# Kernel tuning notes

Measured on AMD Instinct MI355X. Metric: run time of the kernel, lower is better.

## Reference

```python
import jax, jax.numpy as jnp
import numpy as np

N, E, D = 50000, 600000, 128


def setup_inputs() -> dict:
    key = jax.random.key(0)
    ks = jax.random.split(key, 16)
    s = 0.05
    inp = {
        "x": jax.random.normal(ks[0], (N, D), dtype=jnp.float32),
        "Wv": jax.random.normal(ks[1], (D, D), dtype=jnp.float32) * s,
        "bv": jnp.zeros((D,), dtype=jnp.float32),
        "Wa": jax.random.normal(ks[2], (D, D), dtype=jnp.float32) * s,
        "ba": jnp.zeros((D,), dtype=jnp.float32),
        "Wm1": jax.random.normal(ks[3], (D, D), dtype=jnp.float32) * s,
        "bm1": jnp.zeros((D,), dtype=jnp.float32),
        "Wm2": jax.random.normal(ks[4], (D, D), dtype=jnp.float32) * s,
        "bm2": jnp.zeros((D,), dtype=jnp.float32),
        "Wp1": jax.random.normal(ks[5], (D, D), dtype=jnp.float32) * s,
        "bp1": jnp.zeros((D,), dtype=jnp.float32),
        "Wp2": jax.random.normal(ks[6], (D, D), dtype=jnp.float32) * s,
        "bp2": jnp.zeros((D,), dtype=jnp.float32),
        "edge_index": jax.random.randint(ks[7], (2, E), 0, N, dtype=jnp.int64),
        "batch": jnp.zeros((N,), dtype=jnp.int64),
        "passes": 4,
    }
    return inp


def reference(x, Wv, bv, Wa, ba, Wm1, bm1, Wm2, bm2, Wp1, bp1, Wp2, bp2,
              edge_index, batch, passes):
    src, dst = edge_index[0], edge_index[1]
    n = x.shape[0]
    h = x
    for _ in range(passes):
        # gather source features, sum-aggregate at destination nodes
        aggr = jax.ops.segment_sum(h[src], dst, num_segments=n)  # [N, D]
        # update: V(h) + min(h, A(aggr)); V/A are Linear+ReLU (1-layer MLP)
        upd = jax.nn.relu(h @ Wv + bv) + jnp.minimum(h, jax.nn.relu(aggr @ Wa + ba))
        # combine MLP (2 layers: Linear-ReLU-Linear)
        upd = jax.nn.relu(upd @ Wm1 + bm1) @ Wm2 + bm2
        h = jax.nn.relu(upd)
    # final prediction: two stacked Linears, no activation between
    return (h @ Wp1 + bp1) @ Wp2 + bp2
```

## Files before the change

kernel.cpp:

```cpp
#include <hip/hip_runtime.h>

#define D 128

typedef _Float16 half8 __attribute__((ext_vector_type(8)));
typedef float f32x4 __attribute__((ext_vector_type(4)));

__device__ __forceinline__ float frelu(float x) { return fmaxf(x, 0.f); }

__global__ void count_kernel(const int* __restrict__ dst, int E, int* __restrict__ deg) {
    int e = blockIdx.x * blockDim.x + threadIdx.x;
    if (e < E) atomicAdd(&deg[dst[e]], 1);
}

__global__ void scan_partial(const int* __restrict__ deg, int* __restrict__ bsum, int n) {
    __shared__ int red[256];
    int i = blockIdx.x * 256 + threadIdx.x;
    red[threadIdx.x] = (i < n) ? deg[i] : 0;
    __syncthreads();
#pragma unroll
    for (int off = 128; off > 0; off >>= 1) {
        if (threadIdx.x < off) red[threadIdx.x] += red[threadIdx.x + off];
        __syncthreads();
    }
    if (threadIdx.x == 0) bsum[blockIdx.x] = red[0];
}

__global__ void scan_bsum(const int* __restrict__ bsum, int* __restrict__ bpre,
                          int* __restrict__ rowstart, int nb, int n) {
    __shared__ int s[256];
    int t = threadIdx.x;
    int v = (t < nb) ? bsum[t] : 0;
    s[t] = v;
    __syncthreads();
#pragma unroll
    for (int off = 1; off < 256; off <<= 1) {
        int u = 0;
        if (t >= off) u = s[t - off];
        __syncthreads();
        if (t >= off) s[t] += u;
        __syncthreads();
    }
    if (t < nb) bpre[t] = s[t] - v;
    if (t == 255) rowstart[n] = s[255];
}

__global__ void scan_expand(const int* __restrict__ deg, const int* __restrict__ bpre,
                            int* __restrict__ rowstart, int n) {
    __shared__ int s[256];
    int b = blockIdx.x, t = threadIdx.x;
    int i = b * 256 + t;
    int v = (i < n) ? deg[i] : 0;
    s[t] = v;
    __syncthreads();
#pragma unroll
    for (int off = 1; off < 256; off <<= 1) {
        int u = 0;
        if (t >= off) u = s[t - off];
        __syncthreads();
        if (t >= off) s[t] += u;
        __syncthreads();
    }
    if (i < n) rowstart[i] = bpre[b] + s[t] - v;
}

__global__ void fill_kernel(const int* __restrict__ src, const int* __restrict__ dst, int E,
                            const int* __restrict__ rowstart, int* __restrict__ cursor,
                            int* __restrict__ bucket) {
    int e = blockIdx.x * blockDim.x + threadIdx.x;
    if (e < E) {
        int d = dst[e];
        int pos = atomicAdd(&cursor[d], 1);
        bucket[rowstart[d] + pos] = src[e];
    }
}

__global__ void gather_kernel(const float* __restrict__ h, const int* __restrict__ rowstart,
                              const int* __restrict__ bucket, float* __restrict__ aggr, int n) {
    int node = blockIdx.x * 4 + (threadIdx.x >> 6);
    if (node >= n) return;
    int lane = threadIdx.x & 63;
    int col = lane & 31, hf = lane >> 5;
    const float4* __restrict__ h4 = reinterpret_cast<const float4*>(h);
    int s = rowstart[node], e = rowstart[node + 1];
    float4 a[8];
#pragma unroll
    for (int m = 0; m < 8; ++m) a[m] = float4{0.f, 0.f, 0.f, 0.f};
    int j = s;
    for (; j + 16 <= e; j += 16) {
#pragma unroll
        for (int m = 0; m < 8; ++m) {
            float4 v = h4[(size_t)bucket[j + 2 * m + hf] * 32 + col];
            a[m].x += v.x; a[m].y += v.y; a[m].z += v.z; a[m].w += v.w;
        }
    }
    for (; j + 2 <= e; j += 2) {
        float4 v = h4[(size_t)bucket[j + hf] * 32 + col];
        a[0].x += v.x; a[0].y += v.y; a[0].z += v.z; a[0].w += v.w;
    }
    if (j < e && hf == 0) {
        float4 v = h4[(size_t)bucket[j] * 32 + col];
        a[0].x += v.x; a[0].y += v.y; a[0].z += v.z; a[0].w += v.w;
    }
    float4 r;
    r.x = ((a[0].x + a[1].x) + (a[2].x + a[3].x)) + ((a[4].x + a[5].x) + (a[6].x + a[7].x));
    r.y = ((a[0].y + a[1].y) + (a[2].y + a[3].y)) + ((a[4].y + a[5].y) + (a[6].y + a[7].y));
    r.z = ((a[0].z + a[1].z) + (a[2].z + a[3].z)) + ((a[4].z + a[5].z) + (a[6].z + a[7].z));
    r.w = ((a[0].w + a[1].w) + (a[2].w + a[3].w)) + ((a[4].w + a[5].w) + (a[6].w + a[7].w));
    r.x += __shfl(r.x, lane ^ 32);
    r.y += __shfl(r.y, lane ^ 32);
    r.z += __shfl(r.z, lane ^ 32);
    r.w += __shfl(r.w, lane ^ 32);
    if (hf == 0)
        reinterpret_cast<float4*>(aggr)[(size_t)node * 32 + col] = r;
}

__global__ void pack_kernel(const float* __restrict__ W0, const float* __restrict__ W1,
                            const float* __restrict__ W2, const float* __restrict__ W3,
                            const float* __restrict__ W4, const float* __restrict__ W5,
                            _Float16* __restrict__ pk) {
    const float* Ws[6] = {W0, W1, W2, W3, W4, W5};
    const float* __restrict__ W = Ws[blockIdx.x];
    half8* __restrict__ base = reinterpret_cast<half8*>(pk) + (size_t)blockIdx.x * 4096;
    for (int it = threadIdx.x; it < 2048; it += 256) {
        int lane = it & 63, ks = (it >> 6) & 3, cf = it >> 8;
        int c = cf * 16 + (lane & 15);
        half8 hv, lv;
#pragma unroll
        for (int e = 0; e < 8; ++e) {
            int k = ks * 32 + ((e < 4) ? 0 : 16) + (lane >> 4) * 4 + (e & 3);
            float w = W[k * 128 + c];
            _Float16 hi = (_Float16)w;
            hv[e] = hi;
            lv[e] = (_Float16)(w - (float)hi);
        }
        base[(cf * 4 + ks) * 64 + lane] = hv;
        base[2048 + (cf * 4 + ks) * 64 + lane] = lv;
    }
}


__device__ __forceinline__ void split8(const float4 x0, const float4 x1, half8& hh, half8& ll) {
    float xs[8] = {x0.x, x0.y, x0.z, x0.w, x1.x, x1.y, x1.z, x1.w};
#pragma unroll
    for (int e = 0; e < 8; ++e) {
        _Float16 hi = (_Float16)xs[e];
        hh[e] = hi;
        ll[e] = (_Float16)(xs[e] - (float)hi);
    }
}

enum { M_P1, M_P2, M_RELU_BAND, M_RELU_GLOB, M_BIAS_BAND, M_BIAS_GLOB };

#define MFMA(acc, A, B) acc = __builtin_amdgcn_mfma_f32_16x16x32_f16((A), (B), acc, 0, 0, 0)

template <int MODE>
__device__ __forceinline__ void do_cf(int cf,
                                      const half8 ah[4], const half8 al[4],
                                      const half8 bh[4], const half8 bl[4],
                                      float* __restrict__ sB,
                                      const float* __restrict__ bias,
                                      const float* __restrict__ hsrc,
                                      float* __restrict__ gout,
                                      int lane, int band0, int n) {
    const int cl = lane & 15;
    const int lrb = (lane >> 4) * 4;
    f32x4 a0 = {0.f, 0.f, 0.f, 0.f}, a1 = {0.f, 0.f, 0.f, 0.f};
    MFMA(a0, ah[0], bh[0]); MFMA(a0, al[0], bh[0]); MFMA(a0, ah[0], bl[0]); MFMA(a0, al[0], bl[0]);
    MFMA(a0, ah[1], bh[1]); MFMA(a0, al[1], bh[1]); MFMA(a0, ah[1], bl[1]); MFMA(a0, al[1], bl[1]);
    MFMA(a1, ah[2], bh[2]); MFMA(a1, al[2], bh[2]); MFMA(a1, ah[2], bl[2]); MFMA(a1, al[2], bl[2]);
    MFMA(a1, ah[3], bh[3]); MFMA(a1, al[3], bh[3]); MFMA(a1, ah[3], bl[3]); MFMA(a1, al[3], bl[3]);

    const float bb = bias[cf * 16 + cl];
    const int c = cf * 16 + cl;
    const int cq = c >> 2, cr = c & 3;
#pragma unroll
    for (int g = 0; g < 4; ++g) {
        const int r = lrb + g;
        const int slot = cq ^ (r & 7);
        float* __restrict__ addr = &sB[r * 128 + slot * 4 + cr];
        float v = a0[g] + a1[g] + bb;
        if constexpr (MODE == M_P1) {
            *addr = frelu(v);
        } else if constexpr (MODE == M_P2) {
            float u1 = *addr;
            int gr = band0 + r;
            float hv = (gr < n) ? hsrc[(size_t)gr * D + c] : 0.f;
            *addr = frelu(v) + fminf(hv, u1);
        } else if constexpr (MODE == M_RELU_BAND) {
            *addr = frelu(v);
        } else if constexpr (MODE == M_BIAS_BAND) {
            *addr = v;
        } else if constexpr (MODE == M_RELU_GLOB) {
            int gr = band0 + r;
            if (gr < n) gout[(size_t)gr * D + c] = frelu(v);
        } else {
            int gr = band0 + r;
            if (gr < n) gout[(size_t)gr * D + c] = v;
        }
    }
}

template <int MODE, bool A_GLOBAL>
__device__ __forceinline__ void phase(const float4* __restrict__ Ag,
                                      float4* __restrict__ B4,
                                      float* __restrict__ sB,
                                      const half8* __restrict__ pkm,
                                      const float* __restrict__ bias,
                                      const float* __restrict__ hsrc,
                                      float* __restrict__ gout,
                                      int lane, int band0, int n) {
    const int lr = lane & 15;
    const int kb = lane >> 4;

    half8 ah[4], al[4];
    if constexpr (A_GLOBAL) {
        const float4 z = {0.f, 0.f, 0.f, 0.f};
        const int row = band0 + lr;
        const float4* __restrict__ base = Ag + (size_t)row * 32;
        const bool ok = row < n;
#pragma unroll
        for (int ks = 0; ks < 4; ++ks) {
            float4 x0 = ok ? base[ks * 8 + kb] : z;
            float4 x1 = ok ? base[ks * 8 + 4 + kb] : z;
            split8(x0, x1, ah[ks], al[ks]);
        }
    } else {
        const int key = lr & 7;
#pragma unroll
        for (int ks = 0; ks < 4; ++ks) {
            float4 x0 = B4[lr * 32 + ((ks * 8 + kb) ^ key)];
            float4 x1 = B4[lr * 32 + ((ks * 8 + 4 + kb) ^ key)];
            split8(x0, x1, ah[ks], al[ks]);
        }
    }

    const half8* __restrict__ ph = pkm;
    const half8* __restrict__ pl = pkm + 2048;

    half8 bh0[4], bl0[4], bh1[4], bl1[4];
#pragma unroll
    for (int ks = 0; ks < 4; ++ks) {
        bh0[ks] = ph[ks * 64 + lane];
        bl0[ks] = pl[ks * 64 + lane];
    }
#pragma unroll 1
    for (int cf2 = 0; cf2 < 4; ++cf2) {
        const int cfe = cf2 * 2, cfo = cfe + 1;
#pragma unroll
        for (int ks = 0; ks < 4; ++ks) {
            bh1[ks] = ph[(cfo * 4 + ks) * 64 + lane];
            bl1[ks] = pl[(cfo * 4 + ks) * 64 + lane];
        }
        do_cf<MODE>(cfe, ah, al, bh0, bl0, sB, bias, hsrc, gout, lane, band0, n);
        if (cf2 < 3) {
#pragma unroll
            for (int ks = 0; ks < 4; ++ks) {
                bh0[ks] = ph[((cfe + 2) * 4 + ks) * 64 + lane];
                bl0[ks] = pl[((cfe + 2) * 4 + ks) * 64 + lane];
            }
        }
        do_cf<MODE>(cfo, ah, al, bh1, bl1, sB, bias, hsrc, gout, lane, band0, n);
    }
}

__launch_bounds__(64)
__global__ void update_kernel(const float* __restrict__ h, const float* __restrict__ aggr,
                              const _Float16* __restrict__ pk,
                              const float* __restrict__ bv, const float* __restrict__ ba,
                              const float* __restrict__ bm1, const float* __restrict__ bm2,
                              float* __restrict__ hout, int n) {
    __shared__ float4 B4[512];
    float* sB = reinterpret_cast<float*>(B4);
    const int lane = threadIdx.x;
    const int band0 = blockIdx.x * 16;
    const half8* __restrict__ pk8 = reinterpret_cast<const half8*>(pk);
    const float4* __restrict__ h4 = reinterpret_cast<const float4*>(h);
    const float4* __restrict__ a4 = reinterpret_cast<const float4*>(aggr);

    phase<M_P1, true>(a4, B4, sB, pk8 + 0 * 4096, ba, nullptr, nullptr, lane, band0, n);
    phase<M_P2, true>(h4, B4, sB, pk8 + 1 * 4096, bv, h, nullptr, lane, band0, n);
    phase<M_RELU_BAND, false>(nullptr, B4, sB, pk8 + 2 * 4096, bm1, nullptr, nullptr, lane, band0, n);
    phase<M_RELU_GLOB, false>(nullptr, B4, sB, pk8 + 3 * 4096, bm2, nullptr, hout, lane, band0, n);
}

__launch_bounds__(64)
__global__ void final_kernel(const float* __restrict__ h, const _Float16* __restrict__ pk,
                             const float* __restrict__ bp1, const float* __restrict__ bp2,
                             float* __restrict__ out, int n) {
    __shared__ float4 B4[512];
    float* sB = reinterpret_cast<float*>(B4);
    const int lane = threadIdx.x;
    const int band0 = blockIdx.x * 16;
    const half8* __restrict__ pk8 = reinterpret_cast<const half8*>(pk);
    const float4* __restrict__ h4 = reinterpret_cast<const float4*>(h);

    phase<M_BIAS_BAND, true>(h4, B4, sB, pk8 + 4 * 4096, bp1, nullptr, nullptr, lane, band0, n);
    phase<M_BIAS_GLOB, false>(nullptr, B4, sB, pk8 + 5 * 4096, bp2, nullptr, out, lane, band0, n);
}

extern "C" void kernel_launch(void* const* d_in, const int* in_sizes, int n_in,
                              void* d_out, int out_size, void* d_ws, size_t ws_size,
                              hipStream_t stream) {
    const float* x   = (const float*)d_in[0];
    const float* Wv  = (const float*)d_in[1];
    const float* bv  = (const float*)d_in[2];
    const float* Wa  = (const float*)d_in[3];
    const float* ba  = (const float*)d_in[4];
    const float* Wm1 = (const float*)d_in[5];
    const float* bm1 = (const float*)d_in[6];
    const float* Wm2 = (const float*)d_in[7];
    const float* bm2 = (const float*)d_in[8];
    const float* Wp1 = (const float*)d_in[9];
    const float* bp1 = (const float*)d_in[10];
    const float* Wp2 = (const float*)d_in[11];
    const float* bp2 = (const float*)d_in[12];
    const int* ei    = (const int*)d_in[13];

    const int N = in_sizes[0] / D;
    const int E = in_sizes[13] / 2;
    const int* src = ei;
    const int* dst = ei + E;

    char* ws = (char*)d_ws;
    size_t off = 0;
    auto alloc = [&](size_t bytes) -> void* {
        void* p = ws + off;
        off += (bytes + 255) & ~(size_t)255;
        return p;
    };
    float* hb0  = (float*)alloc((size_t)N * D * sizeof(float));
    float* hb1  = (float*)alloc((size_t)N * D * sizeof(float));
    float* aggr = (float*)alloc((size_t)N * D * sizeof(float));
    int* deg      = (int*)alloc((size_t)(N + 1) * sizeof(int));
    int* rowstart = (int*)alloc((size_t)(N + 1) * sizeof(int));
    int* cursor   = (int*)alloc((size_t)(N + 1) * sizeof(int));
    int* bucket   = (int*)alloc((size_t)E * sizeof(int));
    int* bsum     = (int*)alloc(256 * sizeof(int));
    int* bpre     = (int*)alloc(256 * sizeof(int));
    _Float16* pk  = (_Float16*)alloc((size_t)6 * 2 * 128 * 128 * sizeof(_Float16));

    hipMemsetAsync(deg, 0, (size_t)(N + 1) * sizeof(int), stream);
    hipMemsetAsync(cursor, 0, (size_t)(N + 1) * sizeof(int), stream);

    pack_kernel<<<6, 256, 0, stream>>>(Wa, Wv, Wm1, Wm2, Wp1, Wp2, pk);

    int eb = (E + 255) / 256;
    int nb = (N + 255) / 256;
    count_kernel<<<eb, 256, 0, stream>>>(dst, E, deg);
    scan_partial<<<nb, 256, 0, stream>>>(deg, bsum, N);
    scan_bsum<<<1, 256, 0, stream>>>(bsum, bpre, rowstart, nb, N);
    scan_expand<<<nb, 256, 0, stream>>>(deg, bpre, rowstart, N);
    fill_kernel<<<eb, 256, 0, stream>>>(src, dst, E, rowstart, cursor, bucket);

    int ub = (N + 15) / 16;
    int gb = (N + 3) / 4;
    const float* cur = x;
    float* bufs[2] = {hb0, hb1};
    for (int p = 0; p < 4; ++p) {
        gather_kernel<<<gb, 256, 0, stream>>>(cur, rowstart, bucket, aggr, N);
        float* nxt = bufs[p & 1];
        update_kernel<<<ub, 64, 0, stream>>>(cur, aggr, pk, bv, ba, bm1, bm2, nxt, N);
        cur = nxt;
    }
    final_kernel<<<ub, 64, 0, stream>>>(cur, pk, bp1, bp2, (float*)d_out, N);
}
```

Measured before the change: 575.4 us.

## Process two 16-row bands per wavefront to reuse weight fragments across MFMAs

Result: faster. 550.9 us, median of 2 (-4.3%).

```diff
diff --git a/kernel.cpp b/kernel.cpp
--- a/kernel.cpp
+++ b/kernel.cpp
@@ -154,36 +154,27 @@
 #define MFMA(acc, A, B) acc = __builtin_amdgcn_mfma_f32_16x16x32_f16((A), (B), acc, 0, 0, 0)
 
 template <int MODE>
-__device__ __forceinline__ void do_cf(int cf,
-                                      const half8 ah[4], const half8 al[4],
-                                      const half8 bh[4], const half8 bl[4],
-                                      float* __restrict__ sB,
-                                      const float* __restrict__ bias,
-                                      const float* __restrict__ hsrc,
-                                      float* __restrict__ gout,
-                                      int lane, int band0, int n) {
+__device__ __forceinline__ void epi_band(float v4[4], int b, int cf,
+                                         float* __restrict__ sB,
+                                         const float* __restrict__ hsrc,
+                                         float* __restrict__ gout,
+                                         int lane, int row0, int n, float bb) {
     const int cl = lane & 15;
     const int lrb = (lane >> 4) * 4;
-    f32x4 a0 = {0.f, 0.f, 0.f, 0.f}, a1 = {0.f, 0.f, 0.f, 0.f};
-    MFMA(a0, ah[0], bh[0]); MFMA(a0, al[0], bh[0]); MFMA(a0, ah[0], bl[0]); MFMA(a0, al[0], bl[0]);
-    MFMA(a0, ah[1], bh[1]); MFMA(a0, al[1], bh[1]); MFMA(a0, ah[1], bl[1]); MFMA(a0, al[1], bl[1]);
-    MFMA(a1, ah[2], bh[2]); MFMA(a1, al[2], bh[2]); MFMA(a1, ah[2], bl[2]); MFMA(a1, al[2], bl[2]);
-    MFMA(a1, ah[3], bh[3]); MFMA(a1, al[3], bh[3]); MFMA(a1, ah[3], bl[3]); MFMA(a1, al[3], bl[3]);
-
-    const float bb = bias[cf * 16 + cl];
     const int c = cf * 16 + cl;
     const int cq = c >> 2, cr = c & 3;
+    float* __restrict__ sBb = sB + b * 2048;
 #pragma unroll
     for (int g = 0; g < 4; ++g) {
         const int r = lrb + g;
         const int slot = cq ^ (r & 7);
-        float* __restrict__ addr = &sB[r * 128 + slot * 4 + cr];
-        float v = a0[g] + a1[g] + bb;
+        float* __restrict__ addr = &sBb[r * 128 + slot * 4 + cr];
+        float v = v4[g] + bb;
         if constexpr (MODE == M_P1) {
             *addr = frelu(v);
         } else if constexpr (MODE == M_P2) {
             float u1 = *addr;
-            int gr = band0 + r;
+            int gr = row0 + b * 16 + r;
             float hv = (gr < n) ? hsrc[(size_t)gr * D + c] : 0.f;
             *addr = frelu(v) + fminf(hv, u1);
         } else if constexpr (MODE == M_RELU_BAND) {
@@ -191,13 +182,49 @@
         } else if constexpr (MODE == M_BIAS_BAND) {
             *addr = v;
         } else if constexpr (MODE == M_RELU_GLOB) {
-            int gr = band0 + r;
+            int gr = row0 + b * 16 + r;
             if (gr < n) gout[(size_t)gr * D + c] = frelu(v);
         } else {
-            int gr = band0 + r;
+            int gr = row0 + b * 16 + r;
             if (gr < n) gout[(size_t)gr * D + c] = v;
         }
     }
+}
+
+template <int MODE>
+__device__ __forceinline__ void do_cf(int cf,
+                                      const half8 ah0[4], const half8 al0[4],
+                                      const half8 ah1[4], const half8 al1[4],
+                                      const half8 bh[4], const half8 bl[4],
+                                      float* __restrict__ sB,
+                                      const float* __restrict__ bias,
+                                      const float* __restrict__ hsrc,
+                                      float* __restrict__ gout,
+                                      int lane, int row0, int n) {
+    f32x4 p0 = {0.f, 0.f, 0.f, 0.f}, p1 = {0.f, 0.f, 0.f, 0.f};
+    f32x4 q0 = {0.f, 0.f, 0.f, 0.f}, q1 = {0.f, 0.f, 0.f, 0.f};
+    MFMA(p0, ah0[0], bh[0]); MFMA(q0, ah1[0], bh[0]);
+    MFMA(p0, al0[0], bh[0]); MFMA(q0, al1[0], bh[0]);
+    MFMA(p0, ah0[0], bl[0]); MFMA(q0, ah1[0], bl[0]);
+    MFMA(p0, al0[0], bl[0]); MFMA(q0, al1[0], bl[0]);
+    MFMA(p0, ah0[1], bh[1]); MFMA(q0, ah1[1], bh[1]);
+    MFMA(p0, al0[1], bh[1]); MFMA(q0, al1[1], bh[1]);
+    MFMA(p0, ah0[1], bl[1]); MFMA(q0, ah1[1], bl[1]);
+    MFMA(p0, al0[1], bl[1]); MFMA(q0, al1[1], bl[1]);
+    MFMA(p1, ah0[2], bh[2]); MFMA(q1, ah1[2], bh[2]);
+    MFMA(p1, al0[2], bh[2]); MFMA(q1, al1[2], bh[2]);
+    MFMA(p1, ah0[2], bl[2]); MFMA(q1, ah1[2], bl[2]);
+    MFMA(p1, al0[2], bl[2]); MFMA(q1, al1[2], bl[2]);
+    MFMA(p1, ah0[3], bh[3]); MFMA(q1, ah1[3], bh[3]);
+    MFMA(p1, al0[3], bh[3]); MFMA(q1, al1[3], bh[3]);
+    MFMA(p1, ah0[3], bl[3]); MFMA(q1, ah1[3], bl[3]);
+    MFMA(p1, al0[3], bl[3]); MFMA(q1, al1[3], bl[3]);
+
+    const float bb = bias[cf * 16 + (lane & 15)];
+    float v0[4] = {p0[0] + p1[0], p0[1] + p1[1], p0[2] + p1[2], p0[3] + p1[3]};
+    float v1[4] = {q0[0] + q1[0], q0[1] + q1[1], q0[2] + q1[2], q0[3] + q1[3]};
+    epi_band<MODE>(v0, 0, cf, sB, hsrc, gout, lane, row0, n, bb);
+    epi_band<MODE>(v1, 1, cf, sB, hsrc, gout, lane, row0, n, bb);
 }
 
 template <int MODE, bool A_GLOBAL>
@@ -208,21 +235,25 @@
                                       const float* __restrict__ bias,
                                       const float* __restrict__ hsrc,
                                       float* __restrict__ gout,
-                                      int lane, int band0, int n) {
+                                      int lane, int row0, int n) {
     const int lr = lane & 15;
     const int kb = lane >> 4;
 
-    half8 ah[4], al[4];
+    half8 ah0[4], al0[4], ah1[4], al1[4];
     if constexpr (A_GLOBAL) {
         const float4 z = {0.f, 0.f, 0.f, 0.f};
-        const int row = band0 + lr;
-        const float4* __restrict__ base = Ag + (size_t)row * 32;
-        const bool ok = row < n;
+        const int r0 = row0 + lr, r1 = row0 + 16 + lr;
+        const float4* __restrict__ b0 = Ag + (size_t)r0 * 32;
+        const float4* __restrict__ b1 = Ag + (size_t)r1 * 32;
+        const bool ok0 = r0 < n, ok1 = r1 < n;
 #pragma unroll
         for (int ks = 0; ks < 4; ++ks) {
-            float4 x0 = ok ? base[ks * 8 + kb] : z;
-            float4 x1 = ok ? base[ks * 8 + 4 + kb] : z;
-            split8(x0, x1, ah[ks], al[ks]);
+            float4 x0 = ok0 ? b0[ks * 8 + kb] : z;
+            float4 x1 = ok0 ? b0[ks * 8 + 4 + kb] : z;
+            split8(x0, x1, ah0[ks], al0[ks]);
+            float4 y0 = ok1 ? b1[ks * 8 + kb] : z;
+            float4 y1 = ok1 ? b1[ks * 8 + 4 + kb] : z;
+            split8(y0, y1, ah1[ks], al1[ks]);
         }
     } else {
         const int key = lr & 7;
@@ -230,7 +261,10 @@
         for (int ks = 0; ks < 4; ++ks) {
             float4 x0 = B4[lr * 32 + ((ks * 8 + kb) ^ key)];
             float4 x1 = B4[lr * 32 + ((ks * 8 + 4 + kb) ^ key)];
-            split8(x0, x1, ah[ks], al[ks]);
+            split8(x0, x1, ah0[ks], al0[ks]);
+            float4 y0 = B4[512 + lr * 32 + ((ks * 8 + kb) ^ key)];
+            float4 y1 = B4[512 + lr * 32 + ((ks * 8 + 4 + kb) ^ key)];
+            split8(y0, y1, ah1[ks], al1[ks]);
         }
     }
 
@@ -251,7 +285,7 @@
             bh1[ks] = ph[(cfo * 4 + ks) * 64 + lane];
             bl1[ks] = pl[(cfo * 4 + ks) * 64 + lane];
         }
-        do_cf<MODE>(cfe, ah, al, bh0, bl0, sB, bias, hsrc, gout, lane, band0, n);
+        do_cf<MODE>(cfe, ah0, al0, ah1, al1, bh0, bl0, sB, bias, hsrc, gout, lane, row0, n);
         if (cf2 < 3) {
 #pragma unroll
             for (int ks = 0; ks < 4; ++ks) {
@@ -259,7 +293,7 @@
                 bl0[ks] = pl[((cfe + 2) * 4 + ks) * 64 + lane];
             }
         }
-        do_cf<MODE>(cfo, ah, al, bh1, bl1, sB, bias, hsrc, gout, lane, band0, n);
+        do_cf<MODE>(cfo, ah0, al0, ah1, al1, bh1, bl1, sB, bias, hsrc, gout, lane, row0, n);
     }
 }
 
@@ -269,33 +303,33 @@
                               const float* __restrict__ bv, const float* __restrict__ ba,
                               const float* __restrict__ bm1, const float* __restrict__ bm2,
                               float* __restrict__ hout, int n) {
-    __shared__ float4 B4[512];
+    __shared__ float4 B4[1024];
     float* sB = reinterpret_cast<float*>(B4);
     const int lane = threadIdx.x;
-    const int band0 = blockIdx.x * 16;
+    const int row0 = blockIdx.x * 32;
     const half8* __restrict__ pk8 = reinterpret_cast<const half8*>(pk);
     const float4* __restrict__ h4 = reinterpret_cast<const float4*>(h);
     const float4* __restrict__ a4 = reinterpret_cast<const float4*>(aggr);
 
-    phase<M_P1, true>(a4, B4, sB, pk8 + 0 * 4096, ba, nullptr, nullptr, lane, band0, n);
-    phase<M_P2, true>(h4, B4, sB, pk8 + 1 * 4096, bv, h, nullptr, lane, band0, n);
-    phase<M_RELU_BAND, false>(nullptr, B4, sB, pk8 + 2 * 4096, bm1, nullptr, nullptr, lane, band0, n);
-    phase<M_RELU_GLOB, false>(nullptr, B4, sB, pk8 + 3 * 4096, bm2, nullptr, hout, lane, band0, n);
+    phase<M_P1, true>(a4, B4, sB, pk8 + 0 * 4096, ba, nullptr, nullptr, lane, row0, n);
+    phase<M_P2, true>(h4, B4, sB, pk8 + 1 * 4096, bv, h, nullptr, lane, row0, n);
+    phase<M_RELU_BAND, false>(nullptr, B4, sB, pk8 + 2 * 4096, bm1, nullptr, nullptr, lane, row0, n);
+    phase<M_RELU_GLOB, false>(nullptr, B4, sB, pk8 + 3 * 4096, bm2, nullptr, hout, lane, row0, n);
 }
 
 __launch_bounds__(64)
 __global__ void final_kernel(const float* __restrict__ h, const _Float16* __restrict__ pk,
                              const float* __restrict__ bp1, const float* __restrict__ bp2,
                              float* __restrict__ out, int n) {
-    __shared__ float4 B4[512];
+    __shared__ float4 B4[1024];
     float* sB = reinterpret_cast<float*>(B4);
     const int lane = threadIdx.x;
-    const int band0 = blockIdx.x * 16;
+    const int row0 = blockIdx.x * 32;
     const half8* __restrict__ pk8 = reinterpret_cast<const half8*>(pk);
     const float4* __restrict__ h4 = reinterpret_cast<const float4*>(h);
 
-    phase<M_BIAS_BAND, true>(h4, B4, sB, pk8 + 4 * 4096, bp1, nullptr, nullptr, lane, band0, n);
-    phase<M_BIAS_GLOB, false>(nullptr, B4, sB, pk8 + 5 * 4096, bp2, nullptr, out, lane, band0, n);
+    phase<M_BIAS_BAND, true>(h4, B4, sB, pk8 + 4 * 4096, bp1, nullptr, nullptr, lane, row0, n);
+    phase<M_BIAS_GLOB, false>(nullptr, B4, sB, pk8 + 5 * 4096, bp2, nullptr, out, lane, row0, n);
 }
 
 extern "C" void kernel_launch(void* const* d_in, const int* in_sizes, int n_in,
@@ -352,7 +386,7 @@
     scan_expand<<<nb, 256, 0, stream>>>(deg, bpre, rowstart, N);
     fill_kernel<<<eb, 256, 0, stream>>>(src, dst, E, rowstart, cursor, bucket);
 
-    int ub = (N + 15) / 16;
+    int ub = (N + 31) / 32;
     int gb = (N + 3) / 4;
     const float* cur = x;
     float* bufs[2] = {hb0, hb1};
```

## Split each 16-row band's output columns across four waves per block

Applied to the files above, without the earlier changes.

New measurement: 837.2 us. 1.45x slower.

```diff
diff --git a/kernel.cpp b/kernel.cpp
--- a/kernel.cpp
+++ b/kernel.cpp
@@ -157,11 +157,11 @@
 __device__ __forceinline__ void do_cf(int cf,
                                       const half8 ah[4], const half8 al[4],
                                       const half8 bh[4], const half8 bl[4],
-                                      float* __restrict__ sB,
+                                      float* __restrict__ sBw,
                                       const float* __restrict__ bias,
                                       const float* __restrict__ hsrc,
                                       float* __restrict__ gout,
-                                      int lane, int band0, int n) {
+                                      int lane, int row0, int n) {
     const int cl = lane & 15;
     const int lrb = (lane >> 4) * 4;
     f32x4 a0 = {0.f, 0.f, 0.f, 0.f}, a1 = {0.f, 0.f, 0.f, 0.f};
@@ -177,13 +177,13 @@
     for (int g = 0; g < 4; ++g) {
         const int r = lrb + g;
         const int slot = cq ^ (r & 7);
-        float* __restrict__ addr = &sB[r * 128 + slot * 4 + cr];
+        float* __restrict__ addr = &sBw[r * 128 + slot * 4 + cr];
         float v = a0[g] + a1[g] + bb;
         if constexpr (MODE == M_P1) {
             *addr = frelu(v);
         } else if constexpr (MODE == M_P2) {
             float u1 = *addr;
-            int gr = band0 + r;
+            int gr = row0 + r;
             float hv = (gr < n) ? hsrc[(size_t)gr * D + c] : 0.f;
             *addr = frelu(v) + fminf(hv, u1);
         } else if constexpr (MODE == M_RELU_BAND) {
@@ -191,31 +191,31 @@
         } else if constexpr (MODE == M_BIAS_BAND) {
             *addr = v;
         } else if constexpr (MODE == M_RELU_GLOB) {
-            int gr = band0 + r;
+            int gr = row0 + r;
             if (gr < n) gout[(size_t)gr * D + c] = frelu(v);
         } else {
-            int gr = band0 + r;
+            int gr = row0 + r;
             if (gr < n) gout[(size_t)gr * D + c] = v;
         }
     }
 }
 
 template <int MODE, bool A_GLOBAL>
-__device__ __forceinline__ void phase(const float4* __restrict__ Ag,
-                                      float4* __restrict__ B4,
-                                      float* __restrict__ sB,
-                                      const half8* __restrict__ pkm,
-                                      const float* __restrict__ bias,
-                                      const float* __restrict__ hsrc,
-                                      float* __restrict__ gout,
-                                      int lane, int band0, int n) {
+__device__ __forceinline__ void phaseW(const float4* __restrict__ Ag,
+                                       const float4* __restrict__ B4r,
+                                       float* __restrict__ sBw,
+                                       const half8* __restrict__ pkm,
+                                       const float* __restrict__ bias,
+                                       const float* __restrict__ hsrc,
+                                       float* __restrict__ gout,
+                                       int lane, int wv, int row0, int n) {
     const int lr = lane & 15;
     const int kb = lane >> 4;
 
     half8 ah[4], al[4];
     if constexpr (A_GLOBAL) {
         const float4 z = {0.f, 0.f, 0.f, 0.f};
-        const int row = band0 + lr;
+        const int row = row0 + lr;
         const float4* __restrict__ base = Ag + (size_t)row * 32;
         const bool ok = row < n;
 #pragma unroll
@@ -228,74 +228,70 @@
         const int key = lr & 7;
 #pragma unroll
         for (int ks = 0; ks < 4; ++ks) {
-            float4 x0 = B4[lr * 32 + ((ks * 8 + kb) ^ key)];
-            float4 x1 = B4[lr * 32 + ((ks * 8 + 4 + kb) ^ key)];
+            float4 x0 = B4r[lr * 32 + ((ks * 8 + kb) ^ key)];
+            float4 x1 = B4r[lr * 32 + ((ks * 8 + 4 + kb) ^ key)];
             split8(x0, x1, ah[ks], al[ks]);
         }
     }
 
     const half8* __restrict__ ph = pkm;
     const half8* __restrict__ pl = pkm + 2048;
-
-    half8 bh0[4], bl0[4], bh1[4], bl1[4];
+    const int cfA = wv * 2, cfB = cfA + 1;
+
+    half8 bhA[4], blA[4], bhB[4], blB[4];
 #pragma unroll
     for (int ks = 0; ks < 4; ++ks) {
-        bh0[ks] = ph[ks * 64 + lane];
-        bl0[ks] = pl[ks * 64 + lane];
-    }
-#pragma unroll 1
-    for (int cf2 = 0; cf2 < 4; ++cf2) {
-        const int cfe = cf2 * 2, cfo = cfe + 1;
-#pragma unroll
-        for (int ks = 0; ks < 4; ++ks) {
-            bh1[ks] = ph[(cfo * 4 + ks) * 64 + lane];
-            bl1[ks] = pl[(cfo * 4 + ks) * 64 + lane];
-        }
-        do_cf<MODE>(cfe, ah, al, bh0, bl0, sB, bias, hsrc, gout, lane, band0, n);
-        if (cf2 < 3) {
-#pragma unroll
-            for (int ks = 0; ks < 4; ++ks) {
-                bh0[ks] = ph[((cfe + 2) * 4 + ks) * 64 + lane];
-                bl0[ks] = pl[((cfe + 2) * 4 + ks) * 64 + lane];
-            }
-        }
-        do_cf<MODE>(cfo, ah, al, bh1, bl1, sB, bias, hsrc, gout, lane, band0, n);
-    }
-}
-
-__launch_bounds__(64)
+        bhA[ks] = ph[(cfA * 4 + ks) * 64 + lane];
+        blA[ks] = pl[(cfA * 4 + ks) * 64 + lane];
+        bhB[ks] = ph[(cfB * 4 + ks) * 64 + lane];
+        blB[ks] = pl[(cfB * 4 + ks) * 64 + lane];
+    }
+    do_cf<MODE>(cfA, ah, al, bhA, blA, sBw, bias, hsrc, gout, lane, row0, n);
+    do_cf<MODE>(cfB, ah, al, bhB, blB, sBw, bias, hsrc, gout, lane, row0, n);
+}
+
+__launch_bounds__(256)
 __global__ void update_kernel(const float* __restrict__ h, const float* __restrict__ aggr,
                               const _Float16* __restrict__ pk,
                               const float* __restrict__ bv, const float* __restrict__ ba,
                               const float* __restrict__ bm1, const float* __restrict__ bm2,
                               float* __restrict__ hout, int n) {
-    __shared__ float4 B4[512];
-    float* sB = reinterpret_cast<float*>(B4);
-    const int lane = threadIdx.x;
-    const int band0 = blockIdx.x * 16;
+    __shared__ float4 buf1[512];
+    __shared__ float4 buf2[512];
+    float* sB1 = reinterpret_cast<float*>(buf1);
+    float* sB2 = reinterpret_cast<float*>(buf2);
+    const int tid = threadIdx.x;
+    const int lane = tid & 63;
+    const int wv = tid >> 6;
+    const int row0 = blockIdx.x * 16;
     const half8* __restrict__ pk8 = reinterpret_cast<const half8*>(pk);
     const float4* __restrict__ h4 = reinterpret_cast<const float4*>(h);
     const float4* __restrict__ a4 = reinterpret_cast<const float4*>(aggr);
 
-    phase<M_P1, true>(a4, B4, sB, pk8 + 0 * 4096, ba, nullptr, nullptr, lane, band0, n);
-    phase<M_P2, true>(h4, B4, sB, pk8 + 1 * 4096, bv, h, nullptr, lane, band0, n);
-    phase<M_RELU_BAND, false>(nullptr, B4, sB, pk8 + 2 * 4096, bm1, nullptr, nullptr, lane, band0, n);
-    phase<M_RELU_GLOB, false>(nullptr, B4, sB, pk8 + 3 * 4096, bm2, nullptr, hout, lane, band0, n);
-}
-
-__launch_bounds__(64)
+    phaseW<M_P1, true>(a4, nullptr, sB1, pk8 + 0 * 4096, ba, nullptr, nullptr, lane, wv, row0, n);
+    phaseW<M_P2, true>(h4, nullptr, sB1, pk8 + 1 * 4096, bv, h, nullptr, lane, wv, row0, n);
+    __syncthreads();
+    phaseW<M_RELU_BAND, false>(nullptr, buf1, sB2, pk8 + 2 * 4096, bm1, nullptr, nullptr, lane, wv, row0, n);
+    __syncthreads();
+    phaseW<M_RELU_GLOB, false>(nullptr, buf2, nullptr, pk8 + 3 * 4096, bm2, nullptr, hout, lane, wv, row0, n);
+}
+
+__launch_bounds__(256)
 __global__ void final_kernel(const float* __restrict__ h, const _Float16* __restrict__ pk,
                              const float* __restrict__ bp1, const float* __restrict__ bp2,
                              float* __restrict__ out, int n) {
-    __shared__ float4 B4[512];
-    float* sB = reinterpret_cast<float*>(B4);
-    const int lane = threadIdx.x;
-    const int band0 = blockIdx.x * 16;
+    __shared__ float4 buf1[512];
+    float* sB1 = reinterpret_cast<float*>(buf1);
+    const int tid = threadIdx.x;
+    const int lane = tid & 63;
+    const int wv = tid >> 6;
+    const int row0 = blockIdx.x * 16;
     const half8* __restrict__ pk8 = reinterpret_cast<const half8*>(pk);
     const float4* __restrict__ h4 = reinterpret_cast<const float4*>(h);
 
-    phase<M_BIAS_BAND, true>(h4, B4, sB, pk8 + 4 * 4096, bp1, nullptr, nullptr, lane, band0, n);
-    phase<M_BIAS_GLOB, false>(nullptr, B4, sB, pk8 + 5 * 4096, bp2, nullptr, out, lane, band0, n);
+    phaseW<M_BIAS_BAND, true>(h4, nullptr, sB1, pk8 + 4 * 4096, bp1, nullptr, nullptr, lane, wv, row0, n);
+    __syncthreads();
+    phaseW<M_BIAS_GLOB, false>(nullptr, buf1, nullptr, pk8 + 5 * 4096, bp2, nullptr, out, lane, wv, row0, n);
 }
 
 extern "C" void kernel_launch(void* const* d_in, const int* in_sizes, int n_in,
@@ -359,8 +355,8 @@
     for (int p = 0; p < 4; ++p) {
         gather_kernel<<<gb, 256, 0, stream>>>(cur, rowstart, bucket, aggr, N);
         float* nxt = bufs[p & 1];
-        update_kernel<<<ub, 64, 0, stream>>>(cur, aggr, pk, bv, ba, bm1, bm2, nxt, N);
+        update_kernel<<<ub, 256, 0, stream>>>(cur, aggr, pk, bv, ba, bm1, bm2, nxt, N);
         cur = nxt;
     }
-    final_kernel<<<ub, 64, 0, stream>>>(cur, pk, bp1, bp2, (float*)d_out, N);
-}
+    final_kernel<<<ub, 256, 0, stream>>>(cur, pk, bp1, bp2, (float*)d_out, N);
+}
```

## Stage packed weights in LDS and share across eight waves per block

Applied to the files above, without the earlier changes.

New measurement: 592.6 us. 3.0% more time.

```diff
diff --git a/kernel.cpp b/kernel.cpp
--- a/kernel.cpp
+++ b/kernel.cpp
@@ -153,15 +153,21 @@
 
 #define MFMA(acc, A, B) acc = __builtin_amdgcn_mfma_f32_16x16x32_f16((A), (B), acc, 0, 0, 0)
 
+__device__ __forceinline__ void stageW(half8* __restrict__ sW,
+                                       const half8* __restrict__ pkm, int tid) {
+#pragma unroll
+    for (int i = 0; i < 8; ++i) sW[tid + i * 512] = pkm[tid + i * 512];
+}
+
 template <int MODE>
 __device__ __forceinline__ void do_cf(int cf,
                                       const half8 ah[4], const half8 al[4],
                                       const half8 bh[4], const half8 bl[4],
-                                      float* __restrict__ sB,
+                                      float* __restrict__ sBw,
                                       const float* __restrict__ bias,
                                       const float* __restrict__ hsrc,
                                       float* __restrict__ gout,
-                                      int lane, int band0, int n) {
+                                      int lane, int row0, int n) {
     const int cl = lane & 15;
     const int lrb = (lane >> 4) * 4;
     f32x4 a0 = {0.f, 0.f, 0.f, 0.f}, a1 = {0.f, 0.f, 0.f, 0.f};
@@ -177,13 +183,13 @@
     for (int g = 0; g < 4; ++g) {
         const int r = lrb + g;
         const int slot = cq ^ (r & 7);
-        float* __restrict__ addr = &sB[r * 128 + slot * 4 + cr];
+        float* __restrict__ addr = &sBw[r * 128 + slot * 4 + cr];
         float v = a0[g] + a1[g] + bb;
         if constexpr (MODE == M_P1) {
             *addr = frelu(v);
         } else if constexpr (MODE == M_P2) {
             float u1 = *addr;
-            int gr = band0 + r;
+            int gr = row0 + r;
             float hv = (gr < n) ? hsrc[(size_t)gr * D + c] : 0.f;
             *addr = frelu(v) + fminf(hv, u1);
         } else if constexpr (MODE == M_RELU_BAND) {
@@ -191,10 +197,10 @@
         } else if constexpr (MODE == M_BIAS_BAND) {
             *addr = v;
         } else if constexpr (MODE == M_RELU_GLOB) {
-            int gr = band0 + r;
+            int gr = row0 + r;
             if (gr < n) gout[(size_t)gr * D + c] = frelu(v);
         } else {
-            int gr = band0 + r;
+            int gr = row0 + r;
             if (gr < n) gout[(size_t)gr * D + c] = v;
         }
     }
@@ -202,20 +208,20 @@
 
 template <int MODE, bool A_GLOBAL>
 __device__ __forceinline__ void phase(const float4* __restrict__ Ag,
-                                      float4* __restrict__ B4,
+                                      const float4* __restrict__ B4,
                                       float* __restrict__ sB,
-                                      const half8* __restrict__ pkm,
+                                      const half8* __restrict__ sW,
                                       const float* __restrict__ bias,
                                       const float* __restrict__ hsrc,
                                       float* __restrict__ gout,
-                                      int lane, int band0, int n) {
+                                      int lane, int row0, int n) {
     const int lr = lane & 15;
     const int kb = lane >> 4;
 
     half8 ah[4], al[4];
     if constexpr (A_GLOBAL) {
         const float4 z = {0.f, 0.f, 0.f, 0.f};
-        const int row = band0 + lr;
+        const int row = row0 + lr;
         const float4* __restrict__ base = Ag + (size_t)row * 32;
         const bool ok = row < n;
 #pragma unroll
@@ -234,8 +240,8 @@
         }
     }
 
-    const half8* __restrict__ ph = pkm;
-    const half8* __restrict__ pl = pkm + 2048;
+    const half8* __restrict__ ph = sW;
+    const half8* __restrict__ pl = sW + 2048;
 
     half8 bh0[4], bl0[4], bh1[4], bl1[4];
 #pragma unroll
@@ -251,7 +257,7 @@
             bh1[ks] = ph[(cfo * 4 + ks) * 64 + lane];
             bl1[ks] = pl[(cfo * 4 + ks) * 64 + lane];
         }
-        do_cf<MODE>(cfe, ah, al, bh0, bl0, sB, bias, hsrc, gout, lane, band0, n);
+        do_cf<MODE>(cfe, ah, al, bh0, bl0, sB, bias, hsrc, gout, lane, row0, n);
         if (cf2 < 3) {
 #pragma unroll
             for (int ks = 0; ks < 4; ++ks) {
@@ -259,43 +265,67 @@
                 bl0[ks] = pl[((cfe + 2) * 4 + ks) * 64 + lane];
             }
         }
-        do_cf<MODE>(cfo, ah, al, bh1, bl1, sB, bias, hsrc, gout, lane, band0, n);
-    }
-}
-
-__launch_bounds__(64)
+        do_cf<MODE>(cfo, ah, al, bh1, bl1, sB, bias, hsrc, gout, lane, row0, n);
+    }
+}
+
+__launch_bounds__(512)
 __global__ void update_kernel(const float* __restrict__ h, const float* __restrict__ aggr,
                               const _Float16* __restrict__ pk,
                               const float* __restrict__ bv, const float* __restrict__ ba,
                               const float* __restrict__ bm1, const float* __restrict__ bm2,
                               float* __restrict__ hout, int n) {
-    __shared__ float4 B4[512];
-    float* sB = reinterpret_cast<float*>(B4);
-    const int lane = threadIdx.x;
-    const int band0 = blockIdx.x * 16;
+    __shared__ half8 sW[4096];
+    __shared__ float4 sBand[4096];
+    const int tid = threadIdx.x;
+    const int lane = tid & 63;
+    const int wv = tid >> 6;
+    const int row0 = blockIdx.x * 128 + wv * 16;
+    float4* __restrict__ B4 = sBand + wv * 512;
+    float* __restrict__ sB = reinterpret_cast<float*>(B4);
     const half8* __restrict__ pk8 = reinterpret_cast<const half8*>(pk);
     const float4* __restrict__ h4 = reinterpret_cast<const float4*>(h);
     const float4* __restrict__ a4 = reinterpret_cast<const float4*>(aggr);
 
-    phase<M_P1, true>(a4, B4, sB, pk8 + 0 * 4096, ba, nullptr, nullptr, lane, band0, n);
-    phase<M_P2, true>(h4, B4, sB, pk8 + 1 * 4096, bv, h, nullptr, lane, band0, n);
-    phase<M_RELU_BAND, false>(nullptr, B4, sB, pk8 + 2 * 4096, bm1, nullptr, nullptr, lane, band0, n);
-    phase<M_RELU_GLOB, false>(nullptr, B4, sB, pk8 + 3 * 4096, bm2, nullptr, hout, lane, band0, n);
-}
-
-__launch_bounds__(64)
+    stageW(sW, pk8 + 0 * 4096, tid);
+    __syncthreads();
+    phase<M_P1, true>(a4, B4, sB, sW, ba, nullptr, nullptr, lane, row0, n);
+    __syncthreads();
+    stageW(sW, pk8 + 1 * 4096, tid);
+    __syncthreads();
+    phase<M_P2, true>(h4, B4, sB, sW, bv, h, nullptr, lane, row0, n);
+    __syncthreads();
+    stageW(sW, pk8 + 2 * 4096, tid);
+    __syncthreads();
+    phase<M_RELU_BAND, false>(nullptr, B4, sB, sW, bm1, nullptr, nullptr, lane, row0, n);
+    __syncthreads();
+    stageW(sW, pk8 + 3 * 4096, tid);
+    __syncthreads();
+    phase<M_RELU_GLOB, false>(nullptr, B4, sB, sW, bm2, nullptr, hout, lane, row0, n);
+}
+
+__launch_bounds__(512)
 __global__ void final_kernel(const float* __restrict__ h, const _Float16* __restrict__ pk,
                              const float* __restrict__ bp1, const float* __restrict__ bp2,
                              float* __restrict__ out, int n) {
-    __shared__ float4 B4[512];
-    float* sB = reinterpret_cast<float*>(B4);
-    const int lane = threadIdx.x;
-    const int band0 = blockIdx.x * 16;
+    __shared__ half8 sW[4096];
+    __shared__ float4 sBand[4096];
+    const int tid = threadIdx.x;
+    const int lane = tid & 63;
+    const int wv = tid >> 6;
+    const int row0 = blockIdx.x * 128 + wv * 16;
+    float4* __restrict__ B4 = sBand + wv * 512;
+    float* __restrict__ sB = reinterpret_cast<float*>(B4);
     const half8* __restrict__ pk8 = reinterpret_cast<const half8*>(pk);
     const float4* __restrict__ h4 = reinterpret_cast<const float4*>(h);
 
-    phase<M_BIAS_BAND, true>(h4, B4, sB, pk8 + 4 * 4096, bp1, nullptr, nullptr, lane, band0, n);
-    phase<M_BIAS_GLOB, false>(nullptr, B4, sB, pk8 + 5 * 4096, bp2, nullptr, out, lane, band0, n);
+    stageW(sW, pk8 + 4 * 4096, tid);
+    __syncthreads();
+    phase<M_BIAS_BAND, true>(h4, B4, sB, sW, bp1, nullptr, nullptr, lane, row0, n);
+    __syncthreads();
+    stageW(sW, pk8 + 5 * 4096, tid);
+    __syncthreads();
+    phase<M_BIAS_GLOB, false>(nullptr, B4, sB, sW, bp2, nullptr, out, lane, row0, n);
 }
 
 extern "C" void kernel_launch(void* const* d_in, const int* in_sizes, int n_in,
@@ -352,15 +382,15 @@
     scan_expand<<<nb, 256, 0, stream>>>(deg, bpre, rowstart, N);
     fill_kernel<<<eb, 256, 0, stream>>>(src, dst, E, rowstart, cursor, bucket);
 
-    int ub = (N + 15) / 16;
+    int ub = (N + 127) / 128;
     int gb = (N + 3) / 4;
     const float* cur = x;
     float* bufs[2] = {hb0, hb1};
     for (int p = 0; p < 4; ++p) {
         gather_kernel<<<gb, 256, 0, stream>>>(cur, rowstart, bucket, aggr, N);
         float* nxt = bufs[p & 1];
-        update_kernel<<<ub, 64, 0, stream>>>(cur, aggr, pk, bv, ba, bm1, bm2, nxt, N);
+        update_kernel<<<ub, 512, 0, stream>>>(cur, aggr, pk, bv, ba, bm1, bm2, nxt, N);
         cur = nxt;
     }
-    final_kernel<<<ub, 64, 0, stream>>>(cur, pk, bp1, bp2, (float*)d_out, N);
-}
+    final_kernel<<<ub, 512, 0, stream>>>(cur, pk, bp1, bp2, (float*)d_out, N);
+}
```
